# Kernel optimization log

Hardware: AMD Instinct MI355X
Metric: run time of the kernel (lower is better)

The kernel has to match this reference:

```python
import jax, jax.numpy as jnp
import numpy as np

B, F, V, D, ND = 16384, 26, 100000, 64, 13
H1, H2, H3 = 1024, 512, 256


def setup_inputs() -> dict:
    key = jax.random.key(0)
    ks = jax.random.split(key, 12)
    s = 0.02
    return {
        "dense": jax.random.normal(ks[0], (B, ND), jnp.float32),
        "sparse_idx": jax.random.randint(ks[1], (B, F), 0, V),
        "bias": jnp.zeros((1, 1), jnp.float32),
        "emb_tables": jax.random.normal(ks[2], (F, V, D), jnp.float32) * s,
        "lin_tables": jax.random.normal(ks[3], (F, V), jnp.float32) * s,
        "Wd": jax.random.normal(ks[4], (ND, D), jnp.float32) * s,
        "Wld": jax.random.normal(ks[5], (ND, 1), jnp.float32) * s,
        "bld": jnp.zeros((1,), jnp.float32),
        "W1": jax.random.normal(ks[6], ((F + 1) * D, H1), jnp.float32) * s,
        "W2": jax.random.normal(ks[7], (H1, H2), jnp.float32) * s,
        "W3": jax.random.normal(ks[8], (H2, H3), jnp.float32) * s,
        "Wout": jax.random.normal(ks[9], (H3, 1), jnp.float32) * s,
    }


def reference(dense, sparse_idx, bias, emb_tables, lin_tables, Wd, Wld, bld, W1, W2, W3, Wout):
    feat = jnp.arange(F)[None, :]                      # [1,F] broadcasts with idx [B,F]
    sparse_emb = emb_tables[feat, sparse_idx]          # [B,F,D] batched multi-table gather
    dense_emb = dense @ Wd                             # [B,D]
    emb = jnp.concatenate([dense_emb[:, None, :], sparse_emb], axis=1)  # [B,F+1,D]

    # first-order term: linear dense + per-feature 1-dim embeddings
    first = dense @ Wld + bld + lin_tables[feat, sparse_idx].sum(axis=1, keepdims=True)  # [B,1]

    # FM second-order: 0.5 * sum_d ((sum_f e)^2 - sum_f e^2)
    sum_e = emb.sum(axis=1)                            # [B,D]
    second = 0.5 * (sum_e * sum_e - (emb * emb).sum(axis=1)).sum(axis=1, keepdims=True)  # [B,1]

    # deep part (dropout p=0 -> identity)
    h = emb.reshape(emb.shape[0], -1)                  # [B,(F+1)*D]
    h = jax.nn.relu(h @ W1)
    h = jax.nn.relu(h @ W2)
    h = jax.nn.relu(h @ W3)
    deep = h @ Wout                                    # [B,1]

    return bias + first + second + deep
```

## Files before the change

### kernel.cpp

```cpp
#include <hip/hip_runtime.h>
#include <hip/hip_bf16.h>

#define B_SAMP 16384
#define NFEAT 26
#define VOCAB 100000
#define DIM 64
#define NDENSE 13
#define H1 1024
#define H2 512
#define H3 256
#define KIN ((NFEAT + 1) * DIM)
#define KP1 1792

typedef int   i32x4 __attribute__((ext_vector_type(4)));
typedef int   i32x8 __attribute__((ext_vector_type(8)));
typedef float f32x4 __attribute__((ext_vector_type(4)));

__device__ inline void async_load16(const void* g, void* lds) {
  __builtin_amdgcn_global_load_lds(
      (const __attribute__((address_space(1))) void*)g,
      (__attribute__((address_space(3))) void*)lds, 16, 0, 0);
}

__device__ inline unsigned char f32_to_fp8(float v) {
  return (unsigned char)(__builtin_amdgcn_cvt_pk_fp8_f32(v, v, 0, false) & 0xff);
}

__global__ __launch_bounds__(256) void k_embed_fm(
    const float* __restrict__ dense, const int* __restrict__ sidx,
    const float* __restrict__ emb, const float* __restrict__ lin,
    const float* __restrict__ Wd, const float* __restrict__ Wld,
    const float* __restrict__ bld,
    unsigned char* __restrict__ h, float* __restrict__ partial)
{
  int wave = threadIdx.x >> 6, lane = threadIdx.x & 63;
  int b = blockIdx.x * 4 + wave;
  const float* drow = dense + b * NDENSE;

  float de = 0.f;
#pragma unroll
  for (int nd = 0; nd < NDENSE; ++nd) de += drow[nd] * Wd[nd * DIM + lane];

  unsigned char* hrow = h + (size_t)b * KP1;
  hrow[lane] = f32_to_fp8(de);
  hrow[KIN + lane] = 0;
  float sum_e = de, sumsq = de * de;

  float fo = 0.f;
  if (lane < NDENSE) fo = drow[lane] * Wld[lane];

  const int* irow = sidx + b * NFEAT;
#pragma unroll
  for (int f = 0; f < NFEAT; ++f) {
    int ix = irow[f];
    float e = emb[((size_t)f * VOCAB + ix) * DIM + lane];
    sum_e += e; sumsq += e * e;
    hrow[(f + 1) * DIM + lane] = f32_to_fp8(e);
  }
  if (lane < NFEAT) fo += lin[(size_t)lane * VOCAB + irow[lane]];

  float sec = sum_e * sum_e - sumsq;
#pragma unroll
  for (int o = 32; o > 0; o >>= 1) {
    sec += __shfl_down(sec, o);
    fo  += __shfl_down(fo, o);
  }
  if (lane == 0) partial[b] = fo + bld[0] + 0.5f * sec;
}

__global__ __launch_bounds__(256) void k_transpose_fp8(
    const float* __restrict__ src, unsigned char* __restrict__ dst,
    int R, int C, int Rp)
{
  __shared__ float tile[32][33];
  int c0 = blockIdx.x * 32, r0 = blockIdx.y * 32;
  int tx = threadIdx.x & 31, ty = threadIdx.x >> 5;
#pragma unroll
  for (int i = 0; i < 32; i += 8) {
    int r = r0 + ty + i;
    tile[ty + i][tx] = (r < R) ? src[(size_t)r * C + c0 + tx] : 0.f;
  }
  __syncthreads();
#pragma unroll
  for (int i = 0; i < 32; i += 8)
    dst[(size_t)(c0 + ty + i) * Rp + r0 + tx] = f32_to_fp8(tile[tx][ty + i]);
}

template <bool RELU, bool FP8OUT>
__global__ __launch_bounds__(256) void k_gemm_fp8(
    const unsigned char* __restrict__ A,
    const unsigned char* __restrict__ Bt,
    void* __restrict__ Cv, int M, int N, int K)
{
  __shared__ unsigned char As[16384];
  __shared__ unsigned char Bs[16384];
  int tid = threadIdx.x;
  int wave = tid >> 6, lane = tid & 63;
  int wm = wave & 1, wn = wave >> 1;
  int bm = blockIdx.x * 128, bn = blockIdx.y * 128;
  int l15 = lane & 15, quad = lane >> 4;

  f32x4 acc[4][4];
#pragma unroll
  for (int i = 0; i < 4; ++i)
#pragma unroll
    for (int j = 0; j < 4; ++j) acc[i][j] = (f32x4){0.f, 0.f, 0.f, 0.f};

  int nk = K >> 7;
  for (int kt = 0; kt < nk; ++kt) {
    int k0 = kt << 7;
    __syncthreads();
#pragma unroll
    for (int s = 0; s < 2; ++s) {
      int st = 2 * wave + s;
      size_t ga = (size_t)(bm + st * 16 + l15) * K + k0 + quad * 32;
      size_t gb = (size_t)(bn + st * 16 + l15) * K + k0 + quad * 32;
#pragma unroll
      for (int j = 0; j < 2; ++j) {
        async_load16(A + ga + j * 16, &As[st * 2048 + j * 1024]);
        async_load16(Bt + gb + j * 16, &Bs[st * 2048 + j * 1024]);
      }
    }
    __syncthreads();

    i32x8 af[4], bf[4];
#pragma unroll
    for (int i = 0; i < 4; ++i) {
      {
        i32x4 lo = *(const i32x4*)&As[(4 * wm + i) * 2048 + lane * 16];
        i32x4 hi = *(const i32x4*)&As[(4 * wm + i) * 2048 + 1024 + lane * 16];
        af[i] = (i32x8){lo.x, lo.y, lo.z, lo.w, hi.x, hi.y, hi.z, hi.w};
      }
      {
        i32x4 lo = *(const i32x4*)&Bs[(4 * wn + i) * 2048 + lane * 16];
        i32x4 hi = *(const i32x4*)&Bs[(4 * wn + i) * 2048 + 1024 + lane * 16];
        bf[i] = (i32x8){lo.x, lo.y, lo.z, lo.w, hi.x, hi.y, hi.z, hi.w};
      }
    }
#pragma unroll
    for (int mi = 0; mi < 4; ++mi)
#pragma unroll
      for (int ni = 0; ni < 4; ++ni)
        acc[mi][ni] = __builtin_amdgcn_mfma_scale_f32_16x16x128_f8f6f4(
            af[mi], bf[ni], acc[mi][ni],
            0 , 0 , 0, 0x7f7f7f7f, 0, 0x7f7f7f7f);
  }

#pragma unroll
  for (int mi = 0; mi < 4; ++mi)
#pragma unroll
    for (int ni = 0; ni < 4; ++ni)
#pragma unroll
      for (int r = 0; r < 4; ++r) {
        int m = bm + 64 * wm + 16 * mi + quad * 4 + r;
        int n = bn + 64 * wn + 16 * ni + l15;
        float v = acc[mi][ni][r];
        if (RELU) v = fmaxf(v, 0.f);
        if (FP8OUT) ((unsigned char*)Cv)[(size_t)m * N + n] = f32_to_fp8(v);
        else        ((float*)Cv)[(size_t)m * N + n] = v;
      }
}

__global__ __launch_bounds__(256) void k_final(
    const float* __restrict__ a3, const float* __restrict__ wo,
    const float* __restrict__ partial, const float* __restrict__ bias,
    float* __restrict__ out)
{
  int wave = threadIdx.x >> 6, lane = threadIdx.x & 63;
  int b = blockIdx.x * 4 + wave;
  const float* row = a3 + (size_t)b * H3;
  float s = 0.f;
#pragma unroll
  for (int i = 0; i < H3 / 64; ++i)
    s += row[lane + 64 * i] * wo[lane + 64 * i];
#pragma unroll
  for (int o = 32; o > 0; o >>= 1) s += __shfl_down(s, o);
  if (lane == 0) out[b] = bias[0] + partial[b] + s;
}

extern "C" void kernel_launch(void* const* d_in, const int* in_sizes, int n_in,
                              void* d_out, int out_size, void* d_ws, size_t ws_size,
                              hipStream_t stream) {
  const float* dense = (const float*)d_in[0];
  const int*   sidx  = (const int*)d_in[1];
  const float* bias  = (const float*)d_in[2];
  const float* emb   = (const float*)d_in[3];
  const float* lin   = (const float*)d_in[4];
  const float* Wd    = (const float*)d_in[5];
  const float* Wld   = (const float*)d_in[6];
  const float* bld   = (const float*)d_in[7];
  const float* W1    = (const float*)d_in[8];
  const float* W2    = (const float*)d_in[9];
  const float* W3    = (const float*)d_in[10];
  const float* Wout  = (const float*)d_in[11];
  float* out = (float*)d_out;

  char* ws = (char*)d_ws;
  const size_t o_h   = 0;
  const size_t o_a1  = 29360128;
  const size_t o_a2  = 46137344;
  const size_t o_a3  = 54525952;
  const size_t o_w1t = 71303168;
  const size_t o_w2t = 73138176;
  const size_t o_w3t = 73662464;
  const size_t o_par = 73793536;

  unsigned char* h   = (unsigned char*)(ws + o_h);
  unsigned char* a1  = (unsigned char*)(ws + o_a1);
  unsigned char* a2  = (unsigned char*)(ws + o_a2);
  float*         a3  = (float*)(ws + o_a3);
  unsigned char* W1t = (unsigned char*)(ws + o_w1t);
  unsigned char* W2t = (unsigned char*)(ws + o_w2t);
  unsigned char* W3t = (unsigned char*)(ws + o_w3t);
  float* partial     = (float*)(ws + o_par);

  k_transpose_fp8<<<dim3(H1 / 32, KP1 / 32), 256, 0, stream>>>(W1, W1t, KIN, H1, KP1);
  k_transpose_fp8<<<dim3(H2 / 32, H1 / 32), 256, 0, stream>>>(W2, W2t, H1, H2, H1);
  k_transpose_fp8<<<dim3(H3 / 32, H2 / 32), 256, 0, stream>>>(W3, W3t, H2, H3, H2);

  k_embed_fm<<<B_SAMP / 4, 256, 0, stream>>>(dense, sidx, emb, lin, Wd, Wld, bld,
                                             h, partial);

  k_gemm_fp8<true, true ><<<dim3(B_SAMP / 128, H1 / 128), 256, 0, stream>>>(h,  W1t, a1, B_SAMP, H1, KP1);
  k_gemm_fp8<true, true ><<<dim3(B_SAMP / 128, H2 / 128), 256, 0, stream>>>(a1, W2t, a2, B_SAMP, H2, H1);
  k_gemm_fp8<true, false><<<dim3(B_SAMP / 128, H3 / 128), 256, 0, stream>>>(a2, W3t, a3, B_SAMP, H3, H2);

  k_final<<<B_SAMP / 4, 256, 0, stream>>>(a3, Wout, partial, bias, out);
}
```

Measured before the change: 862.5 us.

## Fuse output projection into last GEMM, merge weight transposes, swizzle block order

Merges the three weight transpose launches into one kernel. Fuses the final Wout dot product into the third GEMM epilogue using shuffle reductions and atomicAdd into the output, which the embedding kernel pre-initialises with the bias and first/second-order terms. It also remaps block indices with an XCD-style swizzle. This removes the fp32 a3 round trip and two launches, at the cost of atomic contention and non-deterministic summation order.

```diff
diff --git a/kernel.cpp b/kernel.cpp
--- a/kernel.cpp
+++ b/kernel.cpp
@@ -30,8 +30,8 @@
     const float* __restrict__ dense, const int* __restrict__ sidx,
     const float* __restrict__ emb, const float* __restrict__ lin,
     const float* __restrict__ Wd, const float* __restrict__ Wld,
-    const float* __restrict__ bld,
-    unsigned char* __restrict__ h, float* __restrict__ partial)
+    const float* __restrict__ bld, const float* __restrict__ bias,
+    unsigned char* __restrict__ h, float* __restrict__ out)
 {
   int wave = threadIdx.x >> 6, lane = threadIdx.x & 63;
   int b = blockIdx.x * 4 + wave;
@@ -65,15 +65,22 @@
     sec += __shfl_down(sec, o);
     fo  += __shfl_down(fo, o);
   }
-  if (lane == 0) partial[b] = fo + bld[0] + 0.5f * sec;
-}
-
-__global__ __launch_bounds__(256) void k_transpose_fp8(
-    const float* __restrict__ src, unsigned char* __restrict__ dst,
-    int R, int C, int Rp)
+  if (lane == 0) out[b] = fo + bld[0] + 0.5f * sec + bias[0];
+}
+
+__global__ __launch_bounds__(256) void k_prep_weights(
+    const float* __restrict__ W1, const float* __restrict__ W2,
+    const float* __restrict__ W3,
+    unsigned char* __restrict__ W1t, unsigned char* __restrict__ W2t,
+    unsigned char* __restrict__ W3t)
 {
   __shared__ float tile[32][33];
-  int c0 = blockIdx.x * 32, r0 = blockIdx.y * 32;
+  int id = blockIdx.x;
+  const float* src; unsigned char* dst; int R, C, Rp, bx, by;
+  if (id < 1792)      { src = W1; dst = W1t; R = KIN; C = H1; Rp = KP1; bx = id % 32; by = id / 32; }
+  else if (id < 2304) { id -= 1792; src = W2; dst = W2t; R = H1; C = H2; Rp = H1; bx = id % 16; by = id / 16; }
+  else                { id -= 2304; src = W3; dst = W3t; R = H2; C = H3; Rp = H2; bx = id % 8;  by = id / 8;  }
+  int c0 = bx * 32, r0 = by * 32;
   int tx = threadIdx.x & 31, ty = threadIdx.x >> 5;
 #pragma unroll
   for (int i = 0; i < 32; i += 8) {
@@ -86,18 +93,25 @@
     dst[(size_t)(c0 + ty + i) * Rp + r0 + tx] = f32_to_fp8(tile[tx][ty + i]);
 }
 
-template <bool RELU, bool FP8OUT>
+template <bool RELU, bool FP8OUT, bool REDUCE>
 __global__ __launch_bounds__(256) void k_gemm_fp8(
     const unsigned char* __restrict__ A,
     const unsigned char* __restrict__ Bt,
-    void* __restrict__ Cv, int M, int N, int K)
+    void* __restrict__ Cv, int M, int N, int K,
+    const float* __restrict__ wo, float* __restrict__ outp)
 {
   __shared__ unsigned char As[16384];
   __shared__ unsigned char Bs[16384];
   int tid = threadIdx.x;
   int wave = tid >> 6, lane = tid & 63;
   int wm = wave & 1, wn = wave >> 1;
-  int bm = blockIdx.x * 128, bn = blockIdx.y * 128;
+
+  int gx = gridDim.x, gy = gridDim.y;
+  int wg = blockIdx.y * gx + blockIdx.x;
+  int cpx = (gx * gy) >> 3;
+  int swz = (wg & 7) * cpx + (wg >> 3);
+  int bm = (swz / gy) * 128, bn = (swz % gy) * 128;
+
   int l15 = lane & 15, quad = lane >> 4;
 
   f32x4 acc[4][4];
@@ -146,36 +160,40 @@
             0 , 0 , 0, 0x7f7f7f7f, 0, 0x7f7f7f7f);
   }
 
-#pragma unroll
-  for (int mi = 0; mi < 4; ++mi)
-#pragma unroll
-    for (int ni = 0; ni < 4; ++ni)
+  if (REDUCE) {
+    float wv[4];
+#pragma unroll
+    for (int ni = 0; ni < 4; ++ni) wv[ni] = wo[bn + 64 * wn + 16 * ni + l15];
+#pragma unroll
+    for (int mi = 0; mi < 4; ++mi)
 #pragma unroll
       for (int r = 0; r < 4; ++r) {
-        int m = bm + 64 * wm + 16 * mi + quad * 4 + r;
-        int n = bn + 64 * wn + 16 * ni + l15;
-        float v = acc[mi][ni][r];
-        if (RELU) v = fmaxf(v, 0.f);
-        if (FP8OUT) ((unsigned char*)Cv)[(size_t)m * N + n] = f32_to_fp8(v);
-        else        ((float*)Cv)[(size_t)m * N + n] = v;
-      }
-}
-
-__global__ __launch_bounds__(256) void k_final(
-    const float* __restrict__ a3, const float* __restrict__ wo,
-    const float* __restrict__ partial, const float* __restrict__ bias,
-    float* __restrict__ out)
-{
-  int wave = threadIdx.x >> 6, lane = threadIdx.x & 63;
-  int b = blockIdx.x * 4 + wave;
-  const float* row = a3 + (size_t)b * H3;
-  float s = 0.f;
-#pragma unroll
-  for (int i = 0; i < H3 / 64; ++i)
-    s += row[lane + 64 * i] * wo[lane + 64 * i];
-#pragma unroll
-  for (int o = 32; o > 0; o >>= 1) s += __shfl_down(s, o);
-  if (lane == 0) out[b] = bias[0] + partial[b] + s;
+        float s = 0.f;
+#pragma unroll
+        for (int ni = 0; ni < 4; ++ni)
+          s += fmaxf(acc[mi][ni][r], 0.f) * wv[ni];
+        s += __shfl_xor(s, 1);
+        s += __shfl_xor(s, 2);
+        s += __shfl_xor(s, 4);
+        s += __shfl_xor(s, 8);
+        if (l15 == 0)
+          atomicAdd(outp + bm + 64 * wm + 16 * mi + quad * 4 + r, s);
+      }
+  } else {
+#pragma unroll
+    for (int mi = 0; mi < 4; ++mi)
+#pragma unroll
+      for (int ni = 0; ni < 4; ++ni)
+#pragma unroll
+        for (int r = 0; r < 4; ++r) {
+          int m = bm + 64 * wm + 16 * mi + quad * 4 + r;
+          int n = bn + 64 * wn + 16 * ni + l15;
+          float v = acc[mi][ni][r];
+          if (RELU) v = fmaxf(v, 0.f);
+          if (FP8OUT) ((unsigned char*)Cv)[(size_t)m * N + n] = f32_to_fp8(v);
+          else        ((float*)Cv)[(size_t)m * N + n] = v;
+        }
+  }
 }
 
 extern "C" void kernel_launch(void* const* d_in, const int* in_sizes, int n_in,
@@ -199,31 +217,26 @@
   const size_t o_h   = 0;
   const size_t o_a1  = 29360128;
   const size_t o_a2  = 46137344;
-  const size_t o_a3  = 54525952;
-  const size_t o_w1t = 71303168;
-  const size_t o_w2t = 73138176;
-  const size_t o_w3t = 73662464;
-  const size_t o_par = 73793536;
+  const size_t o_w1t = 54525952;
+  const size_t o_w2t = 56360960;
+  const size_t o_w3t = 56885248;
 
   unsigned char* h   = (unsigned char*)(ws + o_h);
   unsigned char* a1  = (unsigned char*)(ws + o_a1);
   unsigned char* a2  = (unsigned char*)(ws + o_a2);
-  float*         a3  = (float*)(ws + o_a3);
   unsigned char* W1t = (unsigned char*)(ws + o_w1t);
   unsigned char* W2t = (unsigned char*)(ws + o_w2t);
   unsigned char* W3t = (unsigned char*)(ws + o_w3t);
-  float* partial     = (float*)(ws + o_par);
-
-  k_transpose_fp8<<<dim3(H1 / 32, KP1 / 32), 256, 0, stream>>>(W1, W1t, KIN, H1, KP1);
-  k_transpose_fp8<<<dim3(H2 / 32, H1 / 32), 256, 0, stream>>>(W2, W2t, H1, H2, H1);
-  k_transpose_fp8<<<dim3(H3 / 32, H2 / 32), 256, 0, stream>>>(W3, W3t, H2, H3, H2);
+
+  k_prep_weights<<<2432, 256, 0, stream>>>(W1, W2, W3, W1t, W2t, W3t);
 
   k_embed_fm<<<B_SAMP / 4, 256, 0, stream>>>(dense, sidx, emb, lin, Wd, Wld, bld,
-                                             h, partial);
-
-  k_gemm_fp8<true, true ><<<dim3(B_SAMP / 128, H1 / 128), 256, 0, stream>>>(h,  W1t, a1, B_SAMP, H1, KP1);
-  k_gemm_fp8<true, true ><<<dim3(B_SAMP / 128, H2 / 128), 256, 0, stream>>>(a1, W2t, a2, B_SAMP, H2, H1);
-  k_gemm_fp8<true, false><<<dim3(B_SAMP / 128, H3 / 128), 256, 0, stream>>>(a2, W3t, a3, B_SAMP, H3, H2);
-
-  k_final<<<B_SAMP / 4, 256, 0, stream>>>(a3, Wout, partial, bias, out);
-}
+                                             bias, h, out);
+
+  k_gemm_fp8<true, true,  false><<<dim3(B_SAMP / 128, H1 / 128), 256, 0, stream>>>(
+      h,  W1t, a1, B_SAMP, H1, KP1, nullptr, nullptr);
+  k_gemm_fp8<true, true,  false><<<dim3(B_SAMP / 128, H2 / 128), 256, 0, stream>>>(
+      a1, W2t, a2, B_SAMP, H2, H1, nullptr, nullptr);
+  k_gemm_fp8<true, false, true ><<<dim3(B_SAMP / 128, H3 / 128), 256, 0, stream>>>(
+      a2, W3t, nullptr, B_SAMP, H3, H2, Wout, out);
+}
```

Measured after the change: 851.0 us. Within noise of the previous version (-1.3%).
